# Kernel tuning notes

Hardware: AMD Instinct MI355X
Metric: run time of the kernel (lower is better)

The kernel has to match this reference:

```python
import jax, jax.numpy as jnp
import numpy as np

B, N, K = 8, 2048, 32
EPS = 1e-5


def _lrelu(x):
    return jnp.where(x >= 0, x, 0.2 * x)


def _bn(x, p):
    # inference BatchNorm; x: [B, C, ...], p: [4, C] = (gamma, beta, mean, var)
    g, b, m, v = p[0], p[1], p[2], p[3]
    shape = (1, -1) + (1,) * (x.ndim - 2)
    scale = g * jax.lax.rsqrt(v + EPS)
    return (x - m.reshape(shape)) * scale.reshape(shape) + b.reshape(shape)


def _group(x, k):
    # ops.group with xyz_or_feature='feature', feature_or_diff='diff'
    # x: [B, C, N] -> edge features [B, 2C, N, k] = cat(neighbor - center, center)
    xt = jnp.transpose(x, (0, 2, 1))  # [B, N, C]
    sq = jnp.sum(xt * xt, axis=-1)    # [B, N]
    dist = sq[:, :, None] - 2.0 * jnp.einsum('bnc,bmc->bnm', xt, xt) + sq[:, None, :]
    idx = jax.lax.top_k(-dist, k)[1]  # [B, N, k] nearest neighbors
    nbr = jax.vmap(lambda f, i: f[i])(xt, idx)  # [B, N, k, C]
    center = xt[:, :, None, :]
    edge = jnp.concatenate([nbr - center, jnp.broadcast_to(center, nbr.shape)], axis=-1)
    return jnp.transpose(edge, (0, 3, 1, 2))  # [B, 2C, N, k]


def _edgeconv(x, w1, bn1, w2, bn2, k):
    e = _group(x, k)
    h = _lrelu(_bn(jnp.einsum('oc,bcnk->bonk', w1, e), bn1))
    h = _lrelu(_bn(jnp.einsum('oc,bcnk->bonk', w2, h), bn2))
    return jnp.max(h, axis=-1)  # max over neighbors -> [B, C_out, N]


def _model(x,
           ec1_w1, ec1_bn1, ec1_w2, ec1_bn2,
           ec2_w1, ec2_bn1, ec2_w2, ec2_bn2,
           ec3_w1, ec3_bn1, ec3_w2, ec3_bn2,
           emb_w, q_w, k_w, v_w, att_bn1, ff_w1, ff_w2, att_bn2,
           cb_w, cb_bn):
    # EdgeConvBlock (3 stacked EdgeConvs, outputs concatenated)
    f1 = _edgeconv(x, ec1_w1, ec1_bn1, ec1_w2, ec1_bn2, K)
    f2 = _edgeconv(f1, ec2_w1, ec2_bn1, ec2_w2, ec2_bn2, K)
    f3 = _edgeconv(f2, ec3_w1, ec3_bn1, ec3_w2, ec3_bn2, K)
    xc = jnp.concatenate([f1, f2, f3], axis=1)  # [B, 192, N]
    # Point2PointAttentionBlock: embedding then dense self-attention
    h = jnp.einsum('oc,bcn->bon', emb_w, xc)  # [B, 1024, N]
    q = jnp.einsum('oc,bcn->bon', q_w, h)
    kk = jnp.einsum('oc,bcn->bon', k_w, h)
    v = jnp.einsum('oc,bcn->bon', v_w, h)
    scale = jnp.sqrt(jnp.asarray(h.shape[1], h.dtype))
    att = jax.nn.softmax(jnp.einsum('bcn,bcm->bnm', q, kk) / scale, axis=-1)  # [B, N, N]
    x_r = jnp.einsum('bnm,bcm->bcn', att, v)
    h = _bn(h + x_r, att_bn1)
    ff = jnp.einsum('oc,bcn->bon', ff_w2, _lrelu(jnp.einsum('oc,bcn->bon', ff_w1, h)))
    h = _bn(h + ff, att_bn2)
    # ConvBlock head
    return _lrelu(_bn(jnp.einsum('oc,bcn->bon', cb_w, h), cb_bn))  # [B, 1024, N]


def setup_inputs() -> dict:
    key = jax.random.key(0)
    ks = iter(jax.random.split(key, 32))

    def randn(shape, s=0.1):
        return jax.random.normal(next(ks), shape, jnp.float32) * s

    def bnp(c):
        return jax.random.uniform(next(ks), (4, c), jnp.float32, 0.1, 1.0)

    return {
        'x': randn((B, 3, N), 1.0),
        'ec1_w1': randn((64, 6)), 'ec1_bn1': bnp(64),
        'ec1_w2': randn((64, 64)), 'ec1_bn2': bnp(64),
        'ec2_w1': randn((64, 128)), 'ec2_bn1': bnp(64),
        'ec2_w2': randn((64, 64)), 'ec2_bn2': bnp(64),
        'ec3_w1': randn((64, 128)), 'ec3_bn1': bnp(64),
        'ec3_w2': randn((64, 64)), 'ec3_bn2': bnp(64),
        'emb_w': randn((1024, 192), 0.05),
        'q_w': randn((1024, 1024), 0.03),
        'k_w': randn((1024, 1024), 0.03),
        'v_w': randn((1024, 1024), 0.03),
        'att_bn1': bnp(1024),
        'ff_w1': randn((512, 1024), 0.03),
        'ff_w2': randn((1024, 512), 0.03),
        'att_bn2': bnp(1024),
        'cb_w': randn((1024, 1024), 0.03),
        'cb_bn': bnp(1024),
    }


def reference(x,
              ec1_w1, ec1_bn1, ec1_w2, ec1_bn2,
              ec2_w1, ec2_bn1, ec2_w2, ec2_bn2,
              ec3_w1, ec3_bn1, ec3_w2, ec3_bn2,
              emb_w, q_w, k_w, v_w, att_bn1, ff_w1, ff_w2, att_bn2,
              cb_w, cb_bn):
    return _model(x,
                  ec1_w1, ec1_bn1, ec1_w2, ec1_bn2,
                  ec2_w1, ec2_bn1, ec2_w2, ec2_bn2,
                  ec3_w1, ec3_bn1, ec3_w2, ec3_bn2,
                  emb_w, q_w, k_w, v_w, att_bn1, ff_w1, ff_w2, att_bn2,
                  cb_w, cb_bn)
```

## Files before the change

### kernel.cpp

```cpp
#include <hip/hip_runtime.h>
#include <hip/hip_bf16.h>

constexpr int Bn  = 8;
constexpr int Np  = 2048;
constexpr int KNN = 32;

typedef __attribute__((ext_vector_type(8))) short bf16x8;
typedef __attribute__((ext_vector_type(4))) float f32x4;

__device__ static inline void gll16(const void* g, void* l) {
  __builtin_amdgcn_global_load_lds((const __attribute__((address_space(1))) void*)g,
                                   (__attribute__((address_space(3))) void*)l, 16, 0, 0);
}

__device__ static inline unsigned short f2bf(float x) {
  union { __hip_bfloat16 h; unsigned short u; } cv; cv.h = __float2bfloat16(x); return cv.u;
}
__device__ static inline float bf2f(unsigned short u) {
  union { __hip_bfloat16 h; unsigned short u; } cv; cv.u = u; return __bfloat162float(cv.h);
}

__global__ __launch_bounds__(256)
void cvt_bf16_kernel(const float* __restrict__ s, __hip_bfloat16* __restrict__ d, int n) {
  int i = blockIdx.x * 256 + threadIdx.x;
  if (i < n) d[i] = __float2bfloat16(s[i]);
}

template<int CIN, int K1>
__global__ __launch_bounds__(256)
void cvt_w1a(const float* __restrict__ w1, __hip_bfloat16* __restrict__ out) {
  int i = blockIdx.x * 256 + threadIdx.x;
  if (i >= 64 * K1) return;
  int o = i / K1, c = i - o * K1;
  out[i] = __float2bfloat16(c < CIN ? w1[o * 2 * CIN + c] : 0.f);
}

__global__ __launch_bounds__(256)
void xpose_kernel(const float* __restrict__ x, float* __restrict__ xt,
                  __hip_bfloat16* __restrict__ xb) {
  int i = blockIdx.x * 256 + threadIdx.x;
  int b = i >> 11, n = i & 2047;
  const float* p = x + (long)b * 3 * Np + n;
  float vx = p[0], vy = p[Np], vz = p[2 * Np];
  xt[(long)i * 4 + 0] = vx;
  xt[(long)i * 4 + 1] = vy;
  xt[(long)i * 4 + 2] = vz;
  xt[(long)i * 4 + 3] = 0.f;
  __hip_bfloat16* q = xb + (long)i * 8;
  q[0] = __float2bfloat16(vx); q[1] = __float2bfloat16(vy);
  q[2] = __float2bfloat16(vz);
  q[3] = __float2bfloat16(0.f); q[4] = q[3]; q[5] = q[3]; q[6] = q[3]; q[7] = q[3];
}

template<int C, int CP>
__global__ __launch_bounds__(256)
void sq_kernel(const float* __restrict__ f, float* __restrict__ out) {
  int i = blockIdx.x * 256 + threadIdx.x;
  const float* p = f + (long)i * CP;
  float s = 0.f;
#pragma unroll
  for (int c = 0; c < C; ++c) s += p[c] * p[c];
  out[i] = s;
}

__global__ __launch_bounds__(256)
void dist_kernel(const float* __restrict__ A, int lda, long sA,
                 float* __restrict__ C, long sC,
                 const float* __restrict__ sqB, int Kd) {
  int bz = blockIdx.z;
  A += (long)bz * sA;
  C += (long)bz * sC;
  sqB += (long)bz * Np;
  int i0 = blockIdx.y * 128, j0 = blockIdx.x * 128;
  __shared__ float As[8][128];
  __shared__ float Bs[8][128];
  float acc[8][8];
#pragma unroll
  for (int a = 0; a < 8; ++a)
#pragma unroll
    for (int b2 = 0; b2 < 8; ++b2) acc[a][b2] = 0.f;
  int t = threadIdx.x;
  int tx = t & 15, ty = t >> 4;
  for (int k0 = 0; k0 < Kd; k0 += 8) {
    {
      int ii = t >> 1, kk = (t & 1) * 4;
#pragma unroll
      for (int u = 0; u < 4; ++u) {
        int kg = k0 + kk + u;
        As[kk + u][ii] = (kg < Kd) ? A[(long)(i0 + ii) * lda + kg] : 0.f;
        Bs[kk + u][ii] = (kg < Kd) ? A[(long)(j0 + ii) * lda + kg] : 0.f;
      }
    }
    __syncthreads();
#pragma unroll
    for (int kk = 0; kk < 8; ++kk) {
      float av[8], bv[8];
#pragma unroll
      for (int u = 0; u < 8; ++u) av[u] = As[kk][ty * 8 + u];
#pragma unroll
      for (int u = 0; u < 8; ++u) bv[u] = Bs[kk][tx * 8 + u];
#pragma unroll
      for (int a = 0; a < 8; ++a)
#pragma unroll
        for (int b2 = 0; b2 < 8; ++b2) acc[a][b2] += av[a] * bv[b2];
    }
    __syncthreads();
  }
#pragma unroll
  for (int a = 0; a < 8; ++a) {
    int i = i0 + ty * 8 + a;
#pragma unroll
    for (int b2 = 0; b2 < 8; ++b2) {
      int j = j0 + tx * 8 + b2;
      C[(long)i * Np + j] = sqB[j] - 2.f * acc[a][b2];
    }
  }
}


__device__ static inline unsigned umin32(unsigned a, unsigned b) { return a < b ? a : b; }

__device__ static inline unsigned long long shfl64x(unsigned long long k, int m) {
  unsigned lo = (unsigned)__shfl_xor((int)(unsigned)k, m);
  unsigned hi = (unsigned)__shfl_xor((int)(unsigned)(k >> 32), m);
  return ((unsigned long long)hi << 32) | (unsigned long long)lo;
}

__device__ static inline unsigned lane_sort64_u32(unsigned v, int lane) {
#pragma unroll
  for (int k = 2; k <= 64; k <<= 1) {
#pragma unroll
    for (int j = k >> 1; j > 0; j >>= 1) {
      unsigned o = (unsigned)__shfl_xor((int)v, j);
      bool dir = ((lane & k) == 0);
      bool lower = ((lane & j) == 0);
      bool keep = (v < o) == (dir == lower);
      v = keep ? v : o;
    }
  }
  return v;
}

__device__ static inline unsigned long long lane_sort64_u64(unsigned long long v, int lane) {
#pragma unroll
  for (int k = 2; k <= 64; k <<= 1) {
#pragma unroll
    for (int j = k >> 1; j > 0; j >>= 1) {
      unsigned long long o = shfl64x(v, j);
      bool dir = ((lane & k) == 0);
      bool lower = ((lane & j) == 0);
      bool keep = (v < o) == (dir == lower);
      v = keep ? v : o;
    }
  }
  return v;
}

__device__ static inline unsigned long long lane_merge64(unsigned long long a,
                                                         unsigned long long b, int lane) {
  unsigned long long br = shfl64x(b, 63);
  unsigned long long m = a < br ? a : br;
#pragma unroll
  for (int j = 32; j > 0; j >>= 1) {
    unsigned long long o = shfl64x(m, j);
    bool lower = ((lane & j) == 0);
    bool keep = (m < o) == lower;
    m = keep ? m : o;
  }
  return m;
}

__global__ __launch_bounds__(64)
void topk_kernel(const float* __restrict__ D, int* __restrict__ idxOut) {
  long row = (long)blockIdx.y * Np + blockIdx.x;
  const float* rowp = D + row * Np;
  int lane = threadIdx.x;
  __shared__ unsigned long long buf[1024];

  unsigned val[32];
  const float4* rp = (const float4*)rowp;
#pragma unroll
  for (int j4 = 0; j4 < 8; ++j4) {
    float4 f4 = rp[j4 * 64 + lane];
    float fv[4] = {f4.x, f4.y, f4.z, f4.w};
#pragma unroll
    for (int u = 0; u < 4; ++u) {
      unsigned b = __float_as_uint(fv[u]);
      val[j4 * 4 + u] = b ^ ((unsigned)((int)b >> 31) | 0x80000000u);
    }
  }

  unsigned tmn[16];
#pragma unroll
  for (int i = 0; i < 16; ++i) tmn[i] = umin32(val[i], val[i + 16]);
#pragma unroll
  for (int w2 = 8; w2 >= 1; w2 >>= 1)
#pragma unroll
    for (int i = 0; i < 8; ++i)
      if (i < w2) tmn[i] = umin32(tmn[i], tmn[i + w2]);

  unsigned T = (unsigned)__shfl((int)lane_sort64_u32(tmn[0], lane), 31);

  int S = 0;
#pragma unroll
  for (int s = 0; s < 32; ++s) {
    bool p = val[s] <= T;
    unsigned long long mask = __ballot(p);
    int pre = __builtin_amdgcn_mbcnt_hi((unsigned)(mask >> 32),
              __builtin_amdgcn_mbcnt_lo((unsigned)mask, 0u));
    int pos = S + pre;
    if (p && pos < 1024) {
      unsigned idx = (unsigned)((s >> 2) * 256 + lane * 4 + (s & 3));
      buf[pos] = ((unsigned long long)val[s] << 32) | idx;
    }
    S += (int)__popcll(mask);
  }
  __syncthreads();

  unsigned long long cur;
  if (S <= 1024) {
    unsigned long long k0 = (lane < S) ? buf[lane] : ~0ull;
    cur = lane_sort64_u64(k0, lane);
    for (int c = 64; c < S; c += 64) {
      unsigned long long kc = (c + lane < S) ? buf[c + lane] : ~0ull;
      cur = lane_merge64(cur, lane_sort64_u64(kc, lane), lane);
    }
  } else {
    cur = ~0ull;
    for (int s = 0; s < 32; ++s) {
      unsigned idx = (unsigned)((s >> 2) * 256 + lane * 4 + (s & 3));
      unsigned long long kc = ((unsigned long long)val[s] << 32) | idx;
      cur = lane_merge64(cur, lane_sort64_u64(kc, lane), lane);
    }
  }
  if (lane < KNN) idxOut[row * KNN + lane] = (int)(unsigned)cur;
}

template<int CIN, int CP>
__global__ __launch_bounds__(256)
void biasker(const float* __restrict__ feat, const float* __restrict__ w1,
             float* __restrict__ bias) {
  __shared__ float wd[64][CIN + 1];
  int tid = threadIdx.x;
  for (int e = tid; e < 64 * CIN; e += 256) {
    int o = e / CIN, c = e - o * CIN;
    wd[o][c] = w1[o * 2 * CIN + CIN + c] - w1[o * 2 * CIN + c];
  }
  __syncthreads();
  int wv = tid >> 6, o = tid & 63;
  float wr_[CIN];
#pragma unroll
  for (int c = 0; c < CIN; ++c) wr_[c] = wd[o][c];
  long base = (long)blockIdx.y * Np + blockIdx.x * 32 + wv * 8;
  for (int p = 0; p < 8; ++p) {
    const float* fr = feat + (base + p) * CP;
    float acc = 0.f;
#pragma unroll
    for (int c = 0; c < CIN; ++c) acc = fmaf(wr_[c], fr[c], acc);
    bias[(base + p) * 64 + o] = acc;
  }
}

template<int K1>
__global__ __launch_bounds__(256)
void edge_mfma(const __hip_bfloat16* __restrict__ featb, int fstride,
               const int* __restrict__ idx, const float* __restrict__ bias,
               const __hip_bfloat16* __restrict__ w1b,
               const __hip_bfloat16* __restrict__ w2b,
               const float* __restrict__ bn1, const float* __restrict__ bn2,
               float* __restrict__ fout, __hip_bfloat16* __restrict__ xcseg) {
  __shared__ __align__(16) char lds[32768 + 64 * K1 * 2 + 8192 + 1024 + 512];
  __hip_bfloat16* A  = (__hip_bfloat16*)lds;
  __hip_bfloat16* H1 = A + 128 * K1;
  float*          H2 = (float*)lds;
  __hip_bfloat16* W1 = (__hip_bfloat16*)(lds + 32768);
  __hip_bfloat16* W2 = W1 + 64 * K1;
  float* biasS = (float*)(lds + 32768 + 64 * K1 * 2 + 8192);
  int*   idxS  = (int*)(biasS + 256);

  int t = threadIdx.x, lane = t & 63, w = t >> 6;
  long pb = (long)blockIdx.y * Np;
  int p0 = blockIdx.x * 4;

  if (t < 128) idxS[t] = idx[(pb + p0 + (t >> 5)) * KNN + (t & 31)];
  biasS[w * 64 + lane] = bias[(pb + p0 + w) * 64 + lane];
  for (int e = t; e < 64 * K1 / 8; e += 256)
    ((ulonglong2*)W1)[e] = ((const ulonglong2*)w1b)[e];
  for (int e = t; e < 512; e += 256)
    ((ulonglong2*)W2)[e] = ((const ulonglong2*)w2b)[e];
  __syncthreads();

  if (K1 == 64) {
#pragma unroll
    for (int i = 0; i < 4; ++i) {
      int e = t + i * 256;
      int r = e >> 3, cc = e & 7;
      const ulonglong2* src = (const ulonglong2*)(featb + (pb + idxS[r]) * fstride) + cc;
      ((ulonglong2*)(A + r * 64))[cc] = *src;
    }
  } else {
    if (t < 128) {
      int r = t;
      ulonglong2 z; z.x = 0; z.y = 0;
      ((ulonglong2*)(A + r * 32))[0] = *(const ulonglong2*)(featb + (pb + idxS[r]) * fstride);
      ((ulonglong2*)(A + r * 32))[1] = z;
      ((ulonglong2*)(A + r * 32))[2] = z;
      ((ulonglong2*)(A + r * 32))[3] = z;
    }
  }

  int ocol = lane & 15;
  float sc1[4], sh1[4], sc2[4], sh2[4];
#pragma unroll
  for (int jn = 0; jn < 4; ++jn) {
    int o = jn * 16 + ocol;
    sc1[jn] = bn1[o] * rsqrtf(bn1[192 + o] + 1e-5f);
    sh1[jn] = bn1[64 + o] - bn1[128 + o] * sc1[jn];
    sc2[jn] = bn2[o] * rsqrtf(bn2[192 + o] + 1e-5f);
    sh2[jn] = bn2[64 + o] - bn2[128 + o] * sc2[jn];
  }
  __syncthreads();

  int mrow = lane & 15;
  int kc   = (lane >> 4) * 8;
  constexpr int KS = K1 / 32;

  f32x4 acc[2][4];
#pragma unroll
  for (int im = 0; im < 2; ++im)
#pragma unroll
    for (int jn = 0; jn < 4; ++jn) acc[im][jn] = f32x4{0.f, 0.f, 0.f, 0.f};
#pragma unroll
  for (int s = 0; s < KS; ++s) {
    bf16x8 af[2], bf_[4];
#pragma unroll
    for (int im = 0; im < 2; ++im)
      af[im] = *(const bf16x8*)(A + (w * 32 + im * 16 + mrow) * K1 + s * 32 + kc);
#pragma unroll
    for (int jn = 0; jn < 4; ++jn)
      bf_[jn] = *(const bf16x8*)(W1 + (jn * 16 + mrow) * K1 + s * 32 + kc);
#pragma unroll
    for (int im = 0; im < 2; ++im)
#pragma unroll
      for (int jn = 0; jn < 4; ++jn)
        acc[im][jn] = __builtin_amdgcn_mfma_f32_16x16x32_bf16(af[im], bf_[jn], acc[im][jn], 0, 0, 0);
  }
#pragma unroll
  for (int im = 0; im < 2; ++im)
#pragma unroll
    for (int jn = 0; jn < 4; ++jn) {
      int o = jn * 16 + ocol;
      float bsv = biasS[w * 64 + o];
#pragma unroll
      for (int r = 0; r < 4; ++r) {
        int m = w * 32 + im * 16 + (lane >> 4) * 4 + r;
        float x = (acc[im][jn][r] + bsv) * sc1[jn] + sh1[jn];
        x = fmaxf(x, 0.2f * x);
        H1[m * 64 + o] = __float2bfloat16(x);
      }
    }
  __syncthreads();

  bf16x8 a2[2][2], b2[4][2];
#pragma unroll
  for (int im = 0; im < 2; ++im)
#pragma unroll
    for (int s = 0; s < 2; ++s)
      a2[im][s] = *(const bf16x8*)(H1 + (w * 32 + im * 16 + mrow) * 64 + s * 32 + kc);
#pragma unroll
  for (int jn = 0; jn < 4; ++jn)
#pragma unroll
    for (int s = 0; s < 2; ++s)
      b2[jn][s] = *(const bf16x8*)(W2 + (jn * 16 + mrow) * 64 + s * 32 + kc);
  __syncthreads();

  f32x4 acc2[2][4];
#pragma unroll
  for (int im = 0; im < 2; ++im)
#pragma unroll
    for (int jn = 0; jn < 4; ++jn) acc2[im][jn] = f32x4{0.f, 0.f, 0.f, 0.f};
#pragma unroll
  for (int s = 0; s < 2; ++s)
#pragma unroll
    for (int im = 0; im < 2; ++im)
#pragma unroll
      for (int jn = 0; jn < 4; ++jn)
        acc2[im][jn] = __builtin_amdgcn_mfma_f32_16x16x32_bf16(a2[im][s], b2[jn][s], acc2[im][jn], 0, 0, 0);
#pragma unroll
  for (int im = 0; im < 2; ++im)
#pragma unroll
    for (int jn = 0; jn < 4; ++jn) {
      int o = jn * 16 + ocol;
#pragma unroll
      for (int r = 0; r < 4; ++r) {
        int m = w * 32 + im * 16 + (lane >> 4) * 4 + r;
        float x = acc2[im][jn][r] * sc2[jn] + sh2[jn];
        x = fmaxf(x, 0.2f * x);
        H2[m * 64 + o] = x;
      }
    }
  __syncthreads();

  {
    int o = t & 63;
    float m = -3.4e38f;
#pragma unroll
    for (int k = 0; k < 32; ++k) m = fmaxf(m, H2[(w * 32 + k) * 64 + o]);
    int n2 = p0 + w;
    if (fout) fout[(pb + n2) * 64 + o] = m;
    xcseg[(pb + n2) * 192 + o] = __float2bfloat16(m);
  }
}

template<int OUTF, int BNMODE, int RESID, int LRELU>
__global__ __launch_bounds__(256)
void gemm_tn(const __hip_bfloat16* __restrict__ A, int lda, long sA,
             const __hip_bfloat16* __restrict__ B, int ldb, long sB,
             void* __restrict__ Cv, int ldc, long sC,
             const __hip_bfloat16* __restrict__ R, long sR,
             const float* __restrict__ bn, int bnlen, int Kd) {
  int bz = blockIdx.z;
  A += (long)bz * sA;
  B += (long)bz * sB;
  __shared__ __hip_bfloat16 As[128 * 32];
  __shared__ __hip_bfloat16 Bs[128 * 32];
  int t = threadIdx.x, lane = t & 63, w = t >> 6;
  int wm = w & 1, wn = w >> 1;
  long i0 = (long)blockIdx.x * 128, j0 = (long)blockIdx.y * 128;
  f32x4 acc[4][4];
#pragma unroll
  for (int i = 0; i < 4; ++i)
#pragma unroll
    for (int j = 0; j < 4; ++j) acc[i][j] = f32x4{0.f, 0.f, 0.f, 0.f};

  int srow = w * 16 + (lane >> 2);
  int sch  = (lane & 3) * 8;
  const __hip_bfloat16* ga0 = A + (i0 + srow) * lda + sch;
  const __hip_bfloat16* ga1 = A + (i0 + 64 + srow) * lda + sch;
  const __hip_bfloat16* gb0 = B + (j0 + srow) * ldb + sch;
  const __hip_bfloat16* gb1 = B + (j0 + 64 + srow) * ldb + sch;
  __hip_bfloat16* la0 = As + (w * 16) * 32;
  __hip_bfloat16* la1 = As + (64 + w * 16) * 32;
  __hip_bfloat16* lb0 = Bs + (w * 16) * 32;
  __hip_bfloat16* lb1 = Bs + (64 + w * 16) * 32;
  const __hip_bfloat16* pa = As + (wm * 64 + (lane & 15)) * 32 + (lane >> 4) * 8;
  const __hip_bfloat16* pb = Bs + (wn * 64 + (lane & 15)) * 32 + (lane >> 4) * 8;

  for (int k0 = 0; k0 < Kd; k0 += 32) {
    gll16(ga0, la0);
    gll16(ga1, la1);
    gll16(gb0, lb0);
    gll16(gb1, lb1);
    ga0 += 32; ga1 += 32; gb0 += 32; gb1 += 32;
    __syncthreads();
    bf16x8 af[4], bfv[4];
#pragma unroll
    for (int i = 0; i < 4; ++i) af[i]  = *(const bf16x8*)(pa + i * 16 * 32);
#pragma unroll
    for (int j = 0; j < 4; ++j) bfv[j] = *(const bf16x8*)(pb + j * 16 * 32);
#pragma unroll
    for (int i = 0; i < 4; ++i)
#pragma unroll
      for (int j = 0; j < 4; ++j)
        acc[i][j] = __builtin_amdgcn_mfma_f32_16x16x32_bf16(af[i], bfv[j], acc[i][j], 0, 0, 0);
    __syncthreads();
  }

  int mlocal = (lane >> 4) * 4;
  int nlocal = lane & 15;
#pragma unroll
  for (int i = 0; i < 4; ++i) {
    long m0 = i0 + wm * 64 + i * 16 + mlocal;
    float bsc[4], bsh[4];
    if (BNMODE == 1) {
#pragma unroll
      for (int r = 0; r < 4; ++r) {
        long c = m0 + r;
        float sc = bn[c] * rsqrtf(bn[3 * bnlen + c] + 1e-5f);
        bsc[r] = sc;
        bsh[r] = bn[bnlen + c] - bn[2 * bnlen + c] * sc;
      }
    }
#pragma unroll
    for (int j = 0; j < 4; ++j) {
      long nn = j0 + wn * 64 + j * 16 + nlocal;
      float sc2 = 1.f, sh2 = 0.f;
      if (BNMODE == 2) {
        sc2 = bn[nn] * rsqrtf(bn[3 * bnlen + nn] + 1e-5f);
        sh2 = bn[bnlen + nn] - bn[2 * bnlen + nn] * sc2;
      }
      f32x4 v = acc[i][j];
      float o4[4];
      ushort4 rv;
      if (RESID) rv = *(const ushort4*)(R + (long)bz * sR + nn * ldc + m0);
#pragma unroll
      for (int r = 0; r < 4; ++r) {
        float x = v[r];
        if (RESID) x += bf2f(r == 0 ? rv.x : r == 1 ? rv.y : r == 2 ? rv.z : rv.w);
        if (BNMODE == 1) x = x * bsc[r] + bsh[r];
        if (BNMODE == 2) x = x * sc2 + sh2;
        if (LRELU) x = (x >= 0.f) ? x : 0.2f * x;
        o4[r] = x;
      }
      if (OUTF) {
        float* Cp = (float*)Cv + (long)bz * sC + nn * ldc + m0;
        *(float4*)Cp = make_float4(o4[0], o4[1], o4[2], o4[3]);
      } else {
        __hip_bfloat16* Cp = (__hip_bfloat16*)Cv + (long)bz * sC + nn * ldc + m0;
        ushort4 sv;
        sv.x = f2bf(o4[0]); sv.y = f2bf(o4[1]); sv.z = f2bf(o4[2]); sv.w = f2bf(o4[3]);
        *(ushort4*)Cp = sv;
      }
    }
  }
}

template<int OUTF, int BNMODE, int RESID, int LRELU>
__global__ __launch_bounds__(512)
void gemm_db(const __hip_bfloat16* __restrict__ A, int lda, long sA,
             const __hip_bfloat16* __restrict__ B, int ldb, long sB,
             void* __restrict__ Cv, int ldc, long sC,
             const __hip_bfloat16* __restrict__ R, long sR,
             const float* __restrict__ bn, int bnlen, int Kd,
             int gx, int gy) {
  int nwg = gx * gy * Bn;
  int cpx = nwg >> 3;
  int orig = blockIdx.x;
  int wg = (orig & 7) * cpx + (orig >> 3);
  int bz = wg / (gx * gy);
  int rem = wg - bz * (gx * gy);
  int by = rem / gx;
  int bx = rem - by * gx;
  A += (long)bz * sA;
  B += (long)bz * sB;
  long i0 = (long)bx * 256, j0 = (long)by * 256;

  __shared__ __hip_bfloat16 As[2][256 * 64];
  __shared__ __hip_bfloat16 Bs[2][256 * 64];

  int t = threadIdx.x, lane = t & 63, w = t >> 6;
  int wm = w & 1, wn = w >> 1;

  f32x4 acc[8][4];
#pragma unroll
  for (int im = 0; im < 8; ++im)
#pragma unroll
    for (int jn = 0; jn < 4; ++jn) acc[im][jn] = f32x4{0.f, 0.f, 0.f, 0.f};

#define STAGE_DB(bi, kt)                                                     \
  {                                                                          \
    _Pragma("unroll")                                                        \
    for (int i = 0; i < 4; ++i) {                                            \
      int e = t + i * 512;                                                   \
      int r = e >> 3, c = e & 7;                                             \
      int cs = c ^ (r & 7);                                                  \
      gll16(A + (i0 + r) * lda + (kt) * 64 + cs * 8,                         \
            (__hip_bfloat16*)As[bi] + e * 8);                                \
    }                                                                        \
    _Pragma("unroll")                                                        \
    for (int i = 0; i < 4; ++i) {                                            \
      int e = t + i * 512;                                                   \
      int r = e >> 3, c = e & 7;                                             \
      int cs = c ^ (r & 7);                                                  \
      gll16(B + (j0 + r) * ldb + (kt) * 64 + cs * 8,                         \
            (__hip_bfloat16*)Bs[bi] + e * 8);                                \
    }                                                                        \
  }

  int nt = Kd >> 6;
  STAGE_DB(0, 0);
  __syncthreads();

  int cur = 0;
  for (int kt = 0; kt < nt; ++kt) {
    if (kt + 1 < nt) STAGE_DB(cur ^ 1, kt + 1);
    const __hip_bfloat16* Ab = As[cur];
    const __hip_bfloat16* Bb = Bs[cur];
#pragma unroll
    for (int ks = 0; ks < 2; ++ks) {
      bf16x8 af[8], bfv[4];
#pragma unroll
      for (int im = 0; im < 8; ++im) {
        int ra = wm * 128 + im * 16 + (lane & 15);
        int q = (ks * 4 + (lane >> 4)) ^ (ra & 7);
        af[im] = *(const bf16x8*)(Ab + ra * 64 + q * 8);
      }
#pragma unroll
      for (int jn = 0; jn < 4; ++jn) {
        int rb = wn * 64 + jn * 16 + (lane & 15);
        int q = (ks * 4 + (lane >> 4)) ^ (rb & 7);
        bfv[jn] = *(const bf16x8*)(Bb + rb * 64 + q * 8);
      }
#pragma unroll
      for (int im = 0; im < 8; ++im)
#pragma unroll
        for (int jn = 0; jn < 4; ++jn)
          acc[im][jn] = __builtin_amdgcn_mfma_f32_16x16x32_bf16(af[im], bfv[jn], acc[im][jn], 0, 0, 0);
    }
    __syncthreads();
    cur ^= 1;
  }
#undef STAGE_DB

  int mlocal = (lane >> 4) * 4;
  int nlocal = lane & 15;
#pragma unroll
  for (int i = 0; i < 8; ++i) {
    long m0 = i0 + wm * 128 + i * 16 + mlocal;
    float bsc[4], bsh[4];
    if (BNMODE == 1) {
#pragma unroll
      for (int r = 0; r < 4; ++r) {
        long c = m0 + r;
        float sc = bn[c] * rsqrtf(bn[3 * bnlen + c] + 1e-5f);
        bsc[r] = sc;
        bsh[r] = bn[bnlen + c] - bn[2 * bnlen + c] * sc;
      }
    }
#pragma unroll
    for (int j = 0; j < 4; ++j) {
      long nn = j0 + wn * 64 + j * 16 + nlocal;
      float sc2 = 1.f, sh2 = 0.f;
      if (BNMODE == 2) {
        sc2 = bn[nn] * rsqrtf(bn[3 * bnlen + nn] + 1e-5f);
        sh2 = bn[bnlen + nn] - bn[2 * bnlen + nn] * sc2;
      }
      f32x4 v = acc[i][j];
      float o4[4];
      ushort4 rv;
      if (RESID) rv = *(const ushort4*)(R + (long)bz * sR + nn * ldc + m0);
#pragma unroll
      for (int r = 0; r < 4; ++r) {
        float x = v[r];
        if (RESID) x += bf2f(r == 0 ? rv.x : r == 1 ? rv.y : r == 2 ? rv.z : rv.w);
        if (BNMODE == 1) x = x * bsc[r] + bsh[r];
        if (BNMODE == 2) x = x * sc2 + sh2;
        if (LRELU) x = (x >= 0.f) ? x : 0.2f * x;
        o4[r] = x;
      }
      if (OUTF) {
        float* Cp = (float*)Cv + (long)bz * sC + nn * ldc + m0;
        *(float4*)Cp = make_float4(o4[0], o4[1], o4[2], o4[3]);
      } else {
        __hip_bfloat16* Cp = (__hip_bfloat16*)Cv + (long)bz * sC + nn * ldc + m0;
        ushort4 sv;
        sv.x = f2bf(o4[0]); sv.y = f2bf(o4[1]); sv.z = f2bf(o4[2]); sv.w = f2bf(o4[3]);
        *(ushort4*)Cp = sv;
      }
    }
  }
}

__global__ __launch_bounds__(256)
void softmax_bf(__hip_bfloat16* __restrict__ S) {
  long row = (long)blockIdx.y * Np + blockIdx.x;
  __hip_bfloat16* p = S + row * Np;
  int t = threadIdx.x;
  const float scale = 0.03125f;
  float v[8];
  float mx = -3.4e38f;
#pragma unroll
  for (int u = 0; u < 8; ++u) {
    v[u] = __bfloat162float(p[u * 256 + t]) * scale;
    mx = fmaxf(mx, v[u]);
  }
  __shared__ float red[4];
#pragma unroll
  for (int off = 32; off > 0; off >>= 1) mx = fmaxf(mx, __shfl_xor(mx, off));
  if ((t & 63) == 0) red[t >> 6] = mx;
  __syncthreads();
  mx = fmaxf(fmaxf(red[0], red[1]), fmaxf(red[2], red[3]));
  __syncthreads();
  float sum = 0.f;
#pragma unroll
  for (int u = 0; u < 8; ++u) { v[u] = __expf(v[u] - mx); sum += v[u]; }
#pragma unroll
  for (int off = 32; off > 0; off >>= 1) sum += __shfl_xor(sum, off);
  if ((t & 63) == 0) red[t >> 6] = sum;
  __syncthreads();
  sum = red[0] + red[1] + red[2] + red[3];
  float inv = 1.f / sum;
#pragma unroll
  for (int u = 0; u < 8; ++u) p[u * 256 + t] = __float2bfloat16(v[u] * inv);
}

extern "C" void kernel_launch(void* const* d_in, const int* in_sizes, int n_in,
                              void* d_out, int out_size, void* d_ws, size_t ws_size,
                              hipStream_t stream) {
  const float* x       = (const float*)d_in[0];
  const float* ec1_w1  = (const float*)d_in[1];
  const float* ec1_bn1 = (const float*)d_in[2];
  const float* ec1_w2  = (const float*)d_in[3];
  const float* ec1_bn2 = (const float*)d_in[4];
  const float* ec2_w1  = (const float*)d_in[5];
  const float* ec2_bn1 = (const float*)d_in[6];
  const float* ec2_w2  = (const float*)d_in[7];
  const float* ec2_bn2 = (const float*)d_in[8];
  const float* ec3_w1  = (const float*)d_in[9];
  const float* ec3_bn1 = (const float*)d_in[10];
  const float* ec3_w2  = (const float*)d_in[11];
  const float* ec3_bn2 = (const float*)d_in[12];
  const float* emb_w   = (const float*)d_in[13];
  const float* q_w     = (const float*)d_in[14];
  const float* k_w     = (const float*)d_in[15];
  const float* v_w     = (const float*)d_in[16];
  const float* att_bn1 = (const float*)d_in[17];
  const float* ff_w1   = (const float*)d_in[18];
  const float* ff_w2   = (const float*)d_in[19];
  const float* att_bn2 = (const float*)d_in[20];
  const float* cb_w    = (const float*)d_in[21];
  const float* cb_bn   = (const float*)d_in[22];
  float* out = (float*)d_out;
  (void)in_sizes; (void)n_in; (void)out_size; (void)ws_size;

  float* ws  = (float*)d_ws;
  float* xt  = ws;
  float* f1  = xt + 65536;
  float* f2  = f1 + 1048576;
  float* sqb = f2 + 1048576;
  int*   idxb = (int*)(sqb + 16384);
  __hip_bfloat16* xc  = (__hip_bfloat16*)(idxb + 524288);
  __hip_bfloat16* wts = xc + 3145728;
  __hip_bfloat16* ew  = wts + 5439488;
  __hip_bfloat16* xb  = ew + 22528;
  float* big = (float*)(xb + 131072);
  __hip_bfloat16* hb  = (__hip_bfloat16*)big;
  __hip_bfloat16* qb  = hb + 16777216;
  __hip_bfloat16* kb  = qb + 16777216;
  __hip_bfloat16* vtb = kb + 16777216;
  __hip_bfloat16* Sb  = vtb + 16777216;
  float* dist = big;
  float* biasb = big + 33554432;

  __hip_bfloat16* emb_wb = wts;
  __hip_bfloat16* q_wb   = wts + 196608;
  __hip_bfloat16* k_wb   = wts + 1245184;
  __hip_bfloat16* v_wb   = wts + 2293760;
  __hip_bfloat16* ff1_wb = wts + 3342336;
  __hip_bfloat16* ff2_wb = wts + 3866624;
  __hip_bfloat16* cb_wb  = wts + 4390912;

  __hip_bfloat16* w1a1_b = ew;
  __hip_bfloat16* w2_1b  = ew + 2048;
  __hip_bfloat16* w1a2_b = ew + 6144;
  __hip_bfloat16* w2_2b  = ew + 10240;
  __hip_bfloat16* w1a3_b = ew + 14336;
  __hip_bfloat16* w2_3b  = ew + 18432;

  const long sN1024 = (long)Np * 1024;
  const long sN512  = (long)Np * 512;
  const long sN192  = (long)Np * 192;
  const long sNN    = (long)Np * Np;

  cvt_bf16_kernel<<<768,  256, 0, stream>>>(emb_w, emb_wb, 196608);
  cvt_bf16_kernel<<<4096, 256, 0, stream>>>(q_w,   q_wb,   1048576);
  cvt_bf16_kernel<<<4096, 256, 0, stream>>>(k_w,   k_wb,   1048576);
  cvt_bf16_kernel<<<4096, 256, 0, stream>>>(v_w,   v_wb,   1048576);
  cvt_bf16_kernel<<<2048, 256, 0, stream>>>(ff_w1, ff1_wb, 524288);
  cvt_bf16_kernel<<<2048, 256, 0, stream>>>(ff_w2, ff2_wb, 524288);
  cvt_bf16_kernel<<<4096, 256, 0, stream>>>(cb_w,  cb_wb,  1048576);
  cvt_w1a<3, 32><<<8, 256, 0, stream>>>(ec1_w1, w1a1_b);
  cvt_w1a<64, 64><<<16, 256, 0, stream>>>(ec2_w1, w1a2_b);
  cvt_w1a<64, 64><<<16, 256, 0, stream>>>(ec3_w1, w1a3_b);
  cvt_bf16_kernel<<<16, 256, 0, stream>>>(ec1_w2, w2_1b, 4096);
  cvt_bf16_kernel<<<16, 256, 0, stream>>>(ec2_w2, w2_2b, 4096);
  cvt_bf16_kernel<<<16, 256, 0, stream>>>(ec3_w2, w2_3b, 4096);

  xpose_kernel<<<64, 256, 0, stream>>>(x, xt, xb);

  sq_kernel<3, 4><<<64, 256, 0, stream>>>(xt, sqb);
  dist_kernel<<<dim3(16, 16, Bn), 256, 0, stream>>>(xt, 4, (long)Np * 4, dist, sNN, sqb, 3);
  topk_kernel<<<dim3(Np, Bn), 64, 0, stream>>>(dist, idxb);
  biasker<3, 4><<<dim3(Np / 32, Bn), 256, 0, stream>>>(xt, ec1_w1, biasb);
  edge_mfma<32><<<dim3(Np / 4, Bn), 256, 0, stream>>>(
      xb, 8, idxb, biasb, w1a1_b, w2_1b, ec1_bn1, ec1_bn2, f1, xc);

  sq_kernel<64, 64><<<64, 256, 0, stream>>>(f1, sqb);
  dist_kernel<<<dim3(16, 16, Bn), 256, 0, stream>>>(f1, 64, (long)Np * 64, dist, sNN, sqb, 64);
  topk_kernel<<<dim3(Np, Bn), 64, 0, stream>>>(dist, idxb);
  biasker<64, 64><<<dim3(Np / 32, Bn), 256, 0, stream>>>(f1, ec2_w1, biasb);
  edge_mfma<64><<<dim3(Np / 4, Bn), 256, 0, stream>>>(
      xc, 192, idxb, biasb, w1a2_b, w2_2b, ec2_bn1, ec2_bn2, f2, xc + 64);

  sq_kernel<64, 64><<<64, 256, 0, stream>>>(f2, sqb);
  dist_kernel<<<dim3(16, 16, Bn), 256, 0, stream>>>(f2, 64, (long)Np * 64, dist, sNN, sqb, 64);
  topk_kernel<<<dim3(Np, Bn), 64, 0, stream>>>(dist, idxb);
  biasker<64, 64><<<dim3(Np / 32, Bn), 256, 0, stream>>>(f2, ec3_w1, biasb);
  edge_mfma<64><<<dim3(Np / 4, Bn), 256, 0, stream>>>(
      xc + 64, 192, idxb, biasb, w1a3_b, w2_3b, ec3_bn1, ec3_bn2, nullptr, xc + 128);

  gemm_tn<0, 0, 0, 0><<<dim3(8, 16, Bn), 256, 0, stream>>>(
      emb_wb, 192, 0, xc, 192, sN192, hb, 1024, sN1024, nullptr, 0, nullptr, 0, 192);

  gemm_db<0, 0, 0, 0><<<dim3(4 * 8 * Bn), 512, 0, stream>>>(
      q_wb, 1024, 0, hb, 1024, sN1024, qb, 1024, sN1024, nullptr, 0, nullptr, 0, 1024, 4, 8);
  gemm_db<0, 0, 0, 0><<<dim3(4 * 8 * Bn), 512, 0, stream>>>(
      k_wb, 1024, 0, hb, 1024, sN1024, kb, 1024, sN1024, nullptr, 0, nullptr, 0, 1024, 4, 8);
  gemm_db<0, 0, 0, 0><<<dim3(8 * 4 * Bn), 512, 0, stream>>>(
      hb, 1024, sN1024, v_wb, 1024, 0, vtb, 2048, sN1024, nullptr, 0, nullptr, 0, 1024, 8, 4);

  gemm_db<0, 0, 0, 0><<<dim3(8 * 8 * Bn), 512, 0, stream>>>(
      kb, 1024, sN1024, qb, 1024, sN1024, Sb, 2048, sNN, nullptr, 0, nullptr, 0, 1024, 8, 8);
  softmax_bf<<<dim3(Np, Bn), 256, 0, stream>>>(Sb);

  gemm_db<0, 1, 1, 0><<<dim3(4 * 8 * Bn), 512, 0, stream>>>(
      vtb, 2048, sN1024, Sb, 2048, sNN, hb, 1024, sN1024, hb, sN1024, att_bn1, 1024, 2048, 4, 8);

  gemm_tn<0, 0, 0, 1><<<dim3(4, 16, Bn), 256, 0, stream>>>(
      ff1_wb, 1024, 0, hb, 1024, sN1024, qb, 512, sN512, nullptr, 0, nullptr, 0, 1024);
  gemm_db<0, 1, 1, 0><<<dim3(4 * 8 * Bn), 512, 0, stream>>>(
      ff2_wb, 512, 0, qb, 512, sN512, hb, 1024, sN1024, hb, sN1024, att_bn2, 1024, 512, 4, 8);

  gemm_db<1, 2, 0, 1><<<dim3(8 * 4 * Bn), 512, 0, stream>>>(
      hb, 1024, sN1024, cb_wb, 1024, 0, out, 2048, sN1024, nullptr, 0, cb_bn, 1024, 1024, 8, 4);
}
```

Before: 979.0 us.

## Fuse kNN distance and top-k into per-block kernels with split-bf16 MFMA

The separate fp32 distance GEMM and top-k kernels are replaced by fused kNN kernels. These compute distances on-chip and select neighbours without writing the full N×N distance matrix to global memory. For 3-channel input the distances are computed directly from points cached in LDS. For 64-channel features a hi/lo bf16 split with three MFMAs approximates fp32 precision, which could change neighbour ordering near ties. The embedding and ff1 GEMMs also move from gemm_tn to the double-buffered gemm_db kernel.

Measured after the change: 1.013 ms. 1.03x slower.

```diff
diff --git a/kernel.cpp b/kernel.cpp
--- a/kernel.cpp
+++ b/kernel.cpp
@@ -63,60 +63,17 @@
   out[i] = s;
 }
 
-__global__ __launch_bounds__(256)
-void dist_kernel(const float* __restrict__ A, int lda, long sA,
-                 float* __restrict__ C, long sC,
-                 const float* __restrict__ sqB, int Kd) {
-  int bz = blockIdx.z;
-  A += (long)bz * sA;
-  C += (long)bz * sC;
-  sqB += (long)bz * Np;
-  int i0 = blockIdx.y * 128, j0 = blockIdx.x * 128;
-  __shared__ float As[8][128];
-  __shared__ float Bs[8][128];
-  float acc[8][8];
-#pragma unroll
-  for (int a = 0; a < 8; ++a)
-#pragma unroll
-    for (int b2 = 0; b2 < 8; ++b2) acc[a][b2] = 0.f;
-  int t = threadIdx.x;
-  int tx = t & 15, ty = t >> 4;
-  for (int k0 = 0; k0 < Kd; k0 += 8) {
-    {
-      int ii = t >> 1, kk = (t & 1) * 4;
-#pragma unroll
-      for (int u = 0; u < 4; ++u) {
-        int kg = k0 + kk + u;
-        As[kk + u][ii] = (kg < Kd) ? A[(long)(i0 + ii) * lda + kg] : 0.f;
-        Bs[kk + u][ii] = (kg < Kd) ? A[(long)(j0 + ii) * lda + kg] : 0.f;
-      }
-    }
-    __syncthreads();
-#pragma unroll
-    for (int kk = 0; kk < 8; ++kk) {
-      float av[8], bv[8];
-#pragma unroll
-      for (int u = 0; u < 8; ++u) av[u] = As[kk][ty * 8 + u];
-#pragma unroll
-      for (int u = 0; u < 8; ++u) bv[u] = Bs[kk][tx * 8 + u];
-#pragma unroll
-      for (int a = 0; a < 8; ++a)
-#pragma unroll
-        for (int b2 = 0; b2 < 8; ++b2) acc[a][b2] += av[a] * bv[b2];
-    }
-    __syncthreads();
-  }
-#pragma unroll
-  for (int a = 0; a < 8; ++a) {
-    int i = i0 + ty * 8 + a;
-#pragma unroll
-    for (int b2 = 0; b2 < 8; ++b2) {
-      int j = j0 + tx * 8 + b2;
-      C[(long)i * Np + j] = sqB[j] - 2.f * acc[a][b2];
-    }
-  }
-}
-
+template<int CIN, int CP>
+__global__ __launch_bounds__(256)
+void split_kernel(const float* __restrict__ f, __hip_bfloat16* __restrict__ fhi,
+                  __hip_bfloat16* __restrict__ flo) {
+  int i = blockIdx.x * 256 + threadIdx.x;
+  int n = i >> 6, c = i & 63;
+  float v = (c < CIN) ? f[(long)n * CP + c] : 0.f;
+  __hip_bfloat16 h = __float2bfloat16(v);
+  fhi[i] = h;
+  flo[i] = __float2bfloat16(v - __bfloat162float(h));
+}
 
 __device__ static inline unsigned umin32(unsigned a, unsigned b) { return a < b ? a : b; }
 
@@ -170,26 +127,9 @@
   return m;
 }
 
-__global__ __launch_bounds__(64)
-void topk_kernel(const float* __restrict__ D, int* __restrict__ idxOut) {
-  long row = (long)blockIdx.y * Np + blockIdx.x;
-  const float* rowp = D + row * Np;
-  int lane = threadIdx.x;
-  __shared__ unsigned long long buf[1024];
-
-  unsigned val[32];
-  const float4* rp = (const float4*)rowp;
-#pragma unroll
-  for (int j4 = 0; j4 < 8; ++j4) {
-    float4 f4 = rp[j4 * 64 + lane];
-    float fv[4] = {f4.x, f4.y, f4.z, f4.w};
-#pragma unroll
-    for (int u = 0; u < 4; ++u) {
-      unsigned b = __float_as_uint(fv[u]);
-      val[j4 * 4 + u] = b ^ ((unsigned)((int)b >> 31) | 0x80000000u);
-    }
-  }
-
+template<int MAP>
+__device__ static inline void row_topk(const unsigned* val, unsigned long long* cbuf,
+                                       int lane, int* outp) {
   unsigned tmn[16];
 #pragma unroll
   for (int i = 0; i < 16; ++i) tmn[i] = umin32(val[i], val[i + 16]);
@@ -209,31 +149,127 @@
     int pre = __builtin_amdgcn_mbcnt_hi((unsigned)(mask >> 32),
               __builtin_amdgcn_mbcnt_lo((unsigned)mask, 0u));
     int pos = S + pre;
-    if (p && pos < 1024) {
-      unsigned idx = (unsigned)((s >> 2) * 256 + lane * 4 + (s & 3));
-      buf[pos] = ((unsigned long long)val[s] << 32) | idx;
-    }
+    unsigned idx = (MAP == 0) ? (unsigned)((s >> 2) * 256 + lane * 4 + (s & 3))
+                              : (unsigned)((s >> 2) * 256 + (s & 3) * 64 + lane);
+    if (p && pos < 256) cbuf[pos] = ((unsigned long long)val[s] << 32) | idx;
     S += (int)__popcll(mask);
   }
-  __syncthreads();
 
   unsigned long long cur;
-  if (S <= 1024) {
-    unsigned long long k0 = (lane < S) ? buf[lane] : ~0ull;
+  if (S <= 256) {
+    unsigned long long k0 = (lane < S) ? cbuf[lane] : ~0ull;
     cur = lane_sort64_u64(k0, lane);
     for (int c = 64; c < S; c += 64) {
-      unsigned long long kc = (c + lane < S) ? buf[c + lane] : ~0ull;
+      unsigned long long kc = (c + lane < S) ? cbuf[c + lane] : ~0ull;
       cur = lane_merge64(cur, lane_sort64_u64(kc, lane), lane);
     }
   } else {
     cur = ~0ull;
     for (int s = 0; s < 32; ++s) {
-      unsigned idx = (unsigned)((s >> 2) * 256 + lane * 4 + (s & 3));
+      unsigned idx = (MAP == 0) ? (unsigned)((s >> 2) * 256 + lane * 4 + (s & 3))
+                                : (unsigned)((s >> 2) * 256 + (s & 3) * 64 + lane);
       unsigned long long kc = ((unsigned long long)val[s] << 32) | idx;
       cur = lane_merge64(cur, lane_sort64_u64(kc, lane), lane);
     }
   }
-  if (lane < KNN) idxOut[row * KNN + lane] = (int)(unsigned)cur;
+  if (lane < KNN) outp[lane] = (int)(unsigned)cur;
+}
+
+__global__ __launch_bounds__(256)
+void knn3_kernel(const float* __restrict__ xt, const float* __restrict__ sqb,
+                 int* __restrict__ idxOut) {
+  __shared__ float4 F[2048];
+  __shared__ float sqS[2048];
+  __shared__ unsigned long long cbuf[4 * 256];
+  int t = threadIdx.x, lane = t & 63, w = t >> 6;
+  long pb = (long)blockIdx.y * Np;
+  for (int e = t; e < 2048; e += 256) {
+    F[e] = ((const float4*)xt)[pb + e];
+    sqS[e] = sqb[pb + e];
+  }
+  __syncthreads();
+  int row = blockIdx.x * 4 + w;
+  float4 a = F[row];
+  unsigned val[32];
+#pragma unroll
+  for (int j4 = 0; j4 < 8; ++j4)
+#pragma unroll
+    for (int u = 0; u < 4; ++u) {
+      int col = j4 * 256 + u * 64 + lane;
+      float4 fb = F[col];
+      float d = sqS[col] - 2.f * (a.x * fb.x + a.y * fb.y + a.z * fb.z);
+      unsigned b = __float_as_uint(d);
+      val[j4 * 4 + u] = b ^ ((unsigned)((int)b >> 31) | 0x80000000u);
+    }
+  row_topk<1>(val, cbuf + w * 256, lane, idxOut + (pb + row) * KNN);
+}
+
+__global__ __launch_bounds__(256)
+void knn16_kernel(const __hip_bfloat16* __restrict__ fhi,
+                  const __hip_bfloat16* __restrict__ flo,
+                  const float* __restrict__ sqb, int* __restrict__ idxOut) {
+  __shared__ __align__(16) float Dw[16][2048];
+  __shared__ float sqS[2048];
+  __shared__ unsigned long long cbuf[4 * 256];
+  int t = threadIdx.x, lane = t & 63, w = t >> 6;
+  long pb = (long)blockIdx.y * Np;
+  int r0 = blockIdx.x * 16;
+  const __hip_bfloat16* fh = fhi + pb * 64;
+  const __hip_bfloat16* fl = flo + pb * 64;
+
+  for (int e = t; e < 512; e += 256)
+    ((float4*)sqS)[e] = ((const float4*)(sqb + pb))[e];
+
+  int ar = r0 + (lane & 15);
+  int kc = (lane >> 4) * 8;
+  bf16x8 ah[2], al[2];
+#pragma unroll
+  for (int k2 = 0; k2 < 2; ++k2) {
+    ah[k2] = *(const bf16x8*)(fh + (long)ar * 64 + k2 * 32 + kc);
+    al[k2] = *(const bf16x8*)(fl + (long)ar * 64 + k2 * 32 + kc);
+  }
+  __syncthreads();
+
+  for (int ct = 0; ct < 32; ++ct) {
+    int col0 = w * 512 + ct * 16;
+    int bcol = col0 + (lane & 15);
+    bf16x8 bh[2], bl[2];
+#pragma unroll
+    for (int k2 = 0; k2 < 2; ++k2) {
+      bh[k2] = *(const bf16x8*)(fh + (long)bcol * 64 + k2 * 32 + kc);
+      bl[k2] = *(const bf16x8*)(fl + (long)bcol * 64 + k2 * 32 + kc);
+    }
+    f32x4 acc = f32x4{0.f, 0.f, 0.f, 0.f};
+#pragma unroll
+    for (int k2 = 0; k2 < 2; ++k2) {
+      acc = __builtin_amdgcn_mfma_f32_16x16x32_bf16(ah[k2], bh[k2], acc, 0, 0, 0);
+      acc = __builtin_amdgcn_mfma_f32_16x16x32_bf16(ah[k2], bl[k2], acc, 0, 0, 0);
+      acc = __builtin_amdgcn_mfma_f32_16x16x32_bf16(al[k2], bh[k2], acc, 0, 0, 0);
+    }
+    int n = lane & 15, m0 = (lane >> 4) * 4;
+    float sqv = sqS[col0 + n];
+#pragma unroll
+    for (int r = 0; r < 4; ++r)
+      Dw[m0 + r][col0 + n] = sqv - 2.f * acc[r];
+  }
+  __syncthreads();
+
+  for (int rr = 0; rr < 4; ++rr) {
+    int row = w * 4 + rr;
+    unsigned val[32];
+    const float4* rp = (const float4*)&Dw[row][0];
+#pragma unroll
+    for (int j4 = 0; j4 < 8; ++j4) {
+      float4 f4 = rp[j4 * 64 + lane];
+      float fv[4] = {f4.x, f4.y, f4.z, f4.w};
+#pragma unroll
+      for (int u = 0; u < 4; ++u) {
+        unsigned b = __float_as_uint(fv[u]);
+        val[j4 * 4 + u] = b ^ ((unsigned)((int)b >> 31) | 0x80000000u);
+      }
+    }
+    row_topk<0>(val, cbuf + w * 256, lane, idxOut + (pb + r0 + row) * KNN);
+  }
 }
 
 template<int CIN, int CP>
@@ -409,109 +445,6 @@
     int n2 = p0 + w;
     if (fout) fout[(pb + n2) * 64 + o] = m;
     xcseg[(pb + n2) * 192 + o] = __float2bfloat16(m);
-  }
-}
-
-template<int OUTF, int BNMODE, int RESID, int LRELU>
-__global__ __launch_bounds__(256)
-void gemm_tn(const __hip_bfloat16* __restrict__ A, int lda, long sA,
-             const __hip_bfloat16* __restrict__ B, int ldb, long sB,
-             void* __restrict__ Cv, int ldc, long sC,
-             const __hip_bfloat16* __restrict__ R, long sR,
-             const float* __restrict__ bn, int bnlen, int Kd) {
-  int bz = blockIdx.z;
-  A += (long)bz * sA;
-  B += (long)bz * sB;
-  __shared__ __hip_bfloat16 As[128 * 32];
-  __shared__ __hip_bfloat16 Bs[128 * 32];
-  int t = threadIdx.x, lane = t & 63, w = t >> 6;
-  int wm = w & 1, wn = w >> 1;
-  long i0 = (long)blockIdx.x * 128, j0 = (long)blockIdx.y * 128;
-  f32x4 acc[4][4];
-#pragma unroll
-  for (int i = 0; i < 4; ++i)
-#pragma unroll
-    for (int j = 0; j < 4; ++j) acc[i][j] = f32x4{0.f, 0.f, 0.f, 0.f};
-
-  int srow = w * 16 + (lane >> 2);
-  int sch  = (lane & 3) * 8;
-  const __hip_bfloat16* ga0 = A + (i0 + srow) * lda + sch;
-  const __hip_bfloat16* ga1 = A + (i0 + 64 + srow) * lda + sch;
-  const __hip_bfloat16* gb0 = B + (j0 + srow) * ldb + sch;
-  const __hip_bfloat16* gb1 = B + (j0 + 64 + srow) * ldb + sch;
-  __hip_bfloat16* la0 = As + (w * 16) * 32;
-  __hip_bfloat16* la1 = As + (64 + w * 16) * 32;
-  __hip_bfloat16* lb0 = Bs + (w * 16) * 32;
-  __hip_bfloat16* lb1 = Bs + (64 + w * 16) * 32;
-  const __hip_bfloat16* pa = As + (wm * 64 + (lane & 15)) * 32 + (lane >> 4) * 8;
-  const __hip_bfloat16* pb = Bs + (wn * 64 + (lane & 15)) * 32 + (lane >> 4) * 8;
-
-  for (int k0 = 0; k0 < Kd; k0 += 32) {
-    gll16(ga0, la0);
-    gll16(ga1, la1);
-    gll16(gb0, lb0);
-    gll16(gb1, lb1);
-    ga0 += 32; ga1 += 32; gb0 += 32; gb1 += 32;
-    __syncthreads();
-    bf16x8 af[4], bfv[4];
-#pragma unroll
-    for (int i = 0; i < 4; ++i) af[i]  = *(const bf16x8*)(pa + i * 16 * 32);
-#pragma unroll
-    for (int j = 0; j < 4; ++j) bfv[j] = *(const bf16x8*)(pb + j * 16 * 32);
-#pragma unroll
-    for (int i = 0; i < 4; ++i)
-#pragma unroll
-      for (int j = 0; j < 4; ++j)
-        acc[i][j] = __builtin_amdgcn_mfma_f32_16x16x32_bf16(af[i], bfv[j], acc[i][j], 0, 0, 0);
-    __syncthreads();
-  }
-
-  int mlocal = (lane >> 4) * 4;
-  int nlocal = lane & 15;
-#pragma unroll
-  for (int i = 0; i < 4; ++i) {
-    long m0 = i0 + wm * 64 + i * 16 + mlocal;
-    float bsc[4], bsh[4];
-    if (BNMODE == 1) {
-#pragma unroll
-      for (int r = 0; r < 4; ++r) {
-        long c = m0 + r;
-        float sc = bn[c] * rsqrtf(bn[3 * bnlen + c] + 1e-5f);
-        bsc[r] = sc;
-        bsh[r] = bn[bnlen + c] - bn[2 * bnlen + c] * sc;
-      }
-    }
-#pragma unroll
-    for (int j = 0; j < 4; ++j) {
-      long nn = j0 + wn * 64 + j * 16 + nlocal;
-      float sc2 = 1.f, sh2 = 0.f;
-      if (BNMODE == 2) {
-        sc2 = bn[nn] * rsqrtf(bn[3 * bnlen + nn] + 1e-5f);
-        sh2 = bn[bnlen + nn] - bn[2 * bnlen + nn] * sc2;
-      }
-      f32x4 v = acc[i][j];
-      float o4[4];
-      ushort4 rv;
-      if (RESID) rv = *(const ushort4*)(R + (long)bz * sR + nn * ldc + m0);
-#pragma unroll
-      for (int r = 0; r < 4; ++r) {
-        float x = v[r];
-        if (RESID) x += bf2f(r == 0 ? rv.x : r == 1 ? rv.y : r == 2 ? rv.z : rv.w);
-        if (BNMODE == 1) x = x * bsc[r] + bsh[r];
-        if (BNMODE == 2) x = x * sc2 + sh2;
-        if (LRELU) x = (x >= 0.f) ? x : 0.2f * x;
-        o4[r] = x;
-      }
-      if (OUTF) {
-        float* Cp = (float*)Cv + (long)bz * sC + nn * ldc + m0;
-        *(float4*)Cp = make_float4(o4[0], o4[1], o4[2], o4[3]);
-      } else {
-        __hip_bfloat16* Cp = (__hip_bfloat16*)Cv + (long)bz * sC + nn * ldc + m0;
-        ushort4 sv;
-        sv.x = f2bf(o4[0]); sv.y = f2bf(o4[1]); sv.z = f2bf(o4[2]); sv.w = f2bf(o4[3]);
-        *(ushort4*)Cp = sv;
-      }
-    }
   }
 }
 
@@ -729,7 +662,8 @@
   __hip_bfloat16* kb  = qb + 16777216;
   __hip_bfloat16* vtb = kb + 16777216;
   __hip_bfloat16* Sb  = vtb + 16777216;
-  float* dist = big;
+  __hip_bfloat16* fhi = (__hip_bfloat16*)big;
+  __hip_bfloat16* flo = fhi + 1048576;
   float* biasb = big + 33554432;
 
   __hip_bfloat16* emb_wb = wts;
@@ -769,28 +703,27 @@
   xpose_kernel<<<64, 256, 0, stream>>>(x, xt, xb);
 
   sq_kernel<3, 4><<<64, 256, 0, stream>>>(xt, sqb);
-  dist_kernel<<<dim3(16, 16, Bn), 256, 0, stream>>>(xt, 4, (long)Np * 4, dist, sNN, sqb, 3);
-  topk_kernel<<<dim3(Np, Bn), 64, 0, stream>>>(dist, idxb);
+  knn3_kernel<<<dim3(Np / 4, Bn), 256, 0, stream>>>(xt, sqb, idxb);
   biasker<3, 4><<<dim3(Np / 32, Bn), 256, 0, stream>>>(xt, ec1_w1, biasb);
   edge_mfma<32><<<dim3(Np / 4, Bn), 256, 0, stream>>>(
       xb, 8, idxb, biasb, w1a1_b, w2_1b, ec1_bn1, ec1_bn2, f1, xc);
 
   sq_kernel<64, 64><<<64, 256, 0, stream>>>(f1, sqb);
-  dist_kernel<<<dim3(16, 16, Bn), 256, 0, stream>>>(f1, 64, (long)Np * 64, dist, sNN, sqb, 64);
-  topk_kernel<<<dim3(Np, Bn), 64, 0, stream>>>(dist, idxb);
+  split_kernel<64, 64><<<4096, 256, 0, stream>>>(f1, fhi, flo);
+  knn16_kernel<<<dim3(Np / 16, Bn), 256, 0, stream>>>(fhi, flo, sqb, idxb);
   biasker<64, 64><<<dim3(Np / 32, Bn), 256, 0, stream>>>(f1, ec2_w1, biasb);
   edge_mfma<64><<<dim3(Np / 4, Bn), 256, 0, stream>>>(
       xc, 192, idxb, biasb, w1a2_b, w2_2b, ec2_bn1, ec2_bn2, f2, xc + 64);
 
   sq_kernel<64, 64><<<64, 256, 0, stream>>>(f2, sqb);
-  dist_kernel<<<dim3(16, 16, Bn), 256, 0, stream>>>(f2, 64, (long)Np * 64, dist, sNN, sqb, 64);
-  topk_kernel<<<dim3(Np, Bn), 64, 0, stream>>>(dist, idxb);
+  split_kernel<64, 64><<<4096, 256, 0, stream>>>(f2, fhi, flo);
+  knn16_kernel<<<dim3(Np / 16, Bn), 256, 0, stream>>>(fhi, flo, sqb, idxb);
   biasker<64, 64><<<dim3(Np / 32, Bn), 256, 0, stream>>>(f2, ec3_w1, biasb);
   edge_mfma<64><<<dim3(Np / 4, Bn), 256, 0, stream>>>(
       xc + 64, 192, idxb, biasb, w1a3_b, w2_3b, ec3_bn1, ec3_bn2, nullptr, xc + 128);
 
-  gemm_tn<0, 0, 0, 0><<<dim3(8, 16, Bn), 256, 0, stream>>>(
-      emb_wb, 192, 0, xc, 192, sN192, hb, 1024, sN1024, nullptr, 0, nullptr, 0, 192);
+  gemm_db<0, 0, 0, 0><<<dim3(4 * 8 * Bn), 512, 0, stream>>>(
+      emb_wb, 192, 0, xc, 192, sN192, hb, 1024, sN1024, nullptr, 0, nullptr, 0, 192, 4, 8);
 
   gemm_db<0, 0, 0, 0><<<dim3(4 * 8 * Bn), 512, 0, stream>>>(
       q_wb, 1024, 0, hb, 1024, sN1024, qb, 1024, sN1024, nullptr, 0, nullptr, 0, 1024, 4, 8);
@@ -806,8 +739,8 @@
   gemm_db<0, 1, 1, 0><<<dim3(4 * 8 * Bn), 512, 0, stream>>>(
       vtb, 2048, sN1024, Sb, 2048, sNN, hb, 1024, sN1024, hb, sN1024, att_bn1, 1024, 2048, 4, 8);
 
-  gemm_tn<0, 0, 0, 1><<<dim3(4, 16, Bn), 256, 0, stream>>>(
-      ff1_wb, 1024, 0, hb, 1024, sN1024, qb, 512, sN512, nullptr, 0, nullptr, 0, 1024);
+  gemm_db<0, 0, 0, 1><<<dim3(2 * 8 * Bn), 512, 0, stream>>>(
+      ff1_wb, 1024, 0, hb, 1024, sN1024, qb, 512, sN512, nullptr, 0, nullptr, 0, 1024, 2, 8);
   gemm_db<0, 1, 1, 0><<<dim3(4 * 8 * Bn), 512, 0, stream>>>(
       ff2_wb, 512, 0, qb, 512, sN512, hb, 1024, sN1024, hb, sN1024, att_bn2, 1024, 512, 4, 8);
 
```
